# Performance work log

Measured on AMD Instinct MI355X. Metric: run time of the kernel, lower is better.

Reference implementation:

```python
import jax, jax.numpy as jnp
import numpy as np

B, C, H, W = 512, 128, 7, 7
P = 21            # patch_size
DIL = 2           # dilation_patch
PAD = DIL * (P // 2)  # 20: max displacement in pixels


def setup_inputs() -> dict:
    key = jax.random.key(0)
    k1, k2, k3, k4 = jax.random.split(key, 4)
    patch1 = jax.random.normal(k1, (B, C, H, W), jnp.float32)
    patch2 = jax.random.normal(k2, (B, C, H, W), jnp.float32)
    feat = P * P * H * W  # 21609
    w_bbox = jax.random.normal(k3, (4, feat), jnp.float32) * (1.0 / np.sqrt(feat))
    b_bbox = jax.random.normal(k4, (4,), jnp.float32) * 0.01
    return {"patch1": patch1, "patch2": patch2, "w_bbox": w_bbox, "b_bbox": b_bbox}


def _correlation(patch1, patch2):
    """SpatialCorrelationSampler(patch_size=21, dilation_patch=2, kernel_size=1).

    out[b,p,q,i,j] = sum_c patch1[b,c,i,j] * patch2[b,c, i + 2*(p-10), j + 2*(q-10)]
    with zero padding for out-of-bounds displacements. Output: [B, 21, 21, 7, 7].
    """
    padded = jnp.pad(patch2, ((0, 0), (0, 0), (PAD, PAD), (PAD, PAD)))  # [B,C,47,47]
    # Outer product over spatial positions, contracted over channels:
    # T[b,i,j,u,v] = sum_c patch1[b,c,i,j] * padded[b,c,u,v]
    T = jnp.einsum('bcij,bcuv->bijuv', patch1, padded)  # [B,7,7,47,47]
    # Gather the displaced entries: u = 2p + i, v = 2q + j
    Pp, Qq, Ii, Jj = jnp.meshgrid(jnp.arange(P), jnp.arange(P),
                                  jnp.arange(H), jnp.arange(W), indexing='ij')
    corr = T[:, Ii, Jj, DIL * Pp + Ii, DIL * Qq + Jj]  # [B,21,21,7,7]
    return corr


def reference(patch1, patch2, w_bbox, b_bbox):
    corr = _correlation(patch1, patch2)           # [B,21,21,7,7]
    x = corr.reshape(corr.shape[0], -1)           # flatten(start_dim=1)
    return x @ w_bbox.T + b_bbox                  # [B,4]
```

## Files before the change

kernel.cpp:

```cpp
#include <hip/hip_runtime.h>

#define NB    512
#define NC    128
#define HW    49
#define FEAT  21609
#define NPAIR 625
#define CHW   6272
#define NVEC4 1568

__constant__ int c_pi[25]  = {0,0,0,0, 1,1,1, 2,2,2,2, 3,3,3, 4,4,4,4, 5,5,5, 6,6,6,6};
__constant__ int c_pi2[25] = {0,2,4,6, 1,3,5, 0,2,4,6, 1,3,5, 0,2,4,6, 1,3,5, 0,2,4,6};

__global__ __launch_bounds__(256) void corr_head_kernel(
    const float* __restrict__ patch1,
    const float* __restrict__ patch2,
    const float* __restrict__ w_bbox,
    const float* __restrict__ b_bbox,
    float* __restrict__ out)
{
    __shared__ float  s1[CHW];
    __shared__ float  s2[CHW];
    __shared__ float4 s_w[NPAIR];
    __shared__ int    s_pair[NPAIR];
    __shared__ float  s_red[16];

    const int tid = threadIdx.x;
    const int b   = blockIdx.x;

    const float4* g1 = (const float4*)(patch1 + (size_t)b * CHW);
    const float4* g2 = (const float4*)(patch2 + (size_t)b * CHW);
    float4* v1 = (float4*)s1;
    float4* v2 = (float4*)s2;
    for (int t = tid; t < NVEC4; t += 256) {
        v1[t] = g1[t];
        v2[t] = g2[t];
    }

    for (int n = tid; n < NPAIR; n += 256) {
        int a  = n / 25;
        int bb = n - a * 25;
        int i  = c_pi[a],  i2 = c_pi2[a];
        int j  = c_pi[bb], j2 = c_pi2[bb];
        int p  = 10 + ((i2 - i) >> 1);
        int q  = 10 + ((j2 - j) >> 1);
        int feat = ((p * 21 + q) * 7 + i) * 7 + j;
        s_pair[n] = ((i * 7 + j) << 8) | (i2 * 7 + j2);
        s_w[n] = make_float4(w_bbox[feat],
                             w_bbox[FEAT + feat],
                             w_bbox[2 * FEAT + feat],
                             w_bbox[3 * FEAT + feat]);
    }
    __syncthreads();

    float a0 = 0.f, a1 = 0.f, a2 = 0.f, a3 = 0.f;
    for (int n = tid; n < NPAIR; n += 256) {
        int pr = s_pair[n];
        int ij = pr >> 8;
        int kl = pr & 255;
        const float* p1c = s1 + ij;
        const float* p2c = s2 + kl;
        float dot = 0.f;
        #pragma unroll 16
        for (int c = 0; c < NC; ++c)
            dot += p1c[c * HW] * p2c[c * HW];
        float4 w = s_w[n];
        a0 += dot * w.x;
        a1 += dot * w.y;
        a2 += dot * w.z;
        a3 += dot * w.w;
    }

    for (int off = 32; off > 0; off >>= 1) {
        a0 += __shfl_down(a0, off, 64);
        a1 += __shfl_down(a1, off, 64);
        a2 += __shfl_down(a2, off, 64);
        a3 += __shfl_down(a3, off, 64);
    }
    int wave = tid >> 6;
    if ((tid & 63) == 0) {
        s_red[wave * 4 + 0] = a0;
        s_red[wave * 4 + 1] = a1;
        s_red[wave * 4 + 2] = a2;
        s_red[wave * 4 + 3] = a3;
    }
    __syncthreads();
    if (tid < 4) {
        float r = s_red[tid] + s_red[4 + tid] + s_red[8 + tid] + s_red[12 + tid];
        out[b * 4 + tid] = r + b_bbox[tid];
    }
}

extern "C" void kernel_launch(void* const* d_in, const int* in_sizes, int n_in,
                              void* d_out, int out_size, void* d_ws, size_t ws_size,
                              hipStream_t stream) {
    const float* patch1 = (const float*)d_in[0];
    const float* patch2 = (const float*)d_in[1];
    const float* w_bbox = (const float*)d_in[2];
    const float* b_bbox = (const float*)d_in[3];
    float* out = (float*)d_out;
    corr_head_kernel<<<dim3(NB), dim3(256), 0, stream>>>(patch1, patch2, w_bbox, b_bbox, out);
}
```

Baseline: 80.39 us.

## Transpose patches to channel-contiguous smem and split channels across lanes

```diff
diff --git a/kernel.cpp b/kernel.cpp
--- a/kernel.cpp
+++ b/kernel.cpp
@@ -4,12 +4,11 @@
 #define NC    128
 #define HW    49
 #define FEAT  21609
-#define NPAIR 625
 #define CHW   6272
-#define NVEC4 1568
+#define NV4   1568
+#define TSTR  132
 
-__constant__ int c_pi[25]  = {0,0,0,0, 1,1,1, 2,2,2,2, 3,3,3, 4,4,4,4, 5,5,5, 6,6,6,6};
-__constant__ int c_pi2[25] = {0,2,4,6, 1,3,5, 0,2,4,6, 1,3,5, 0,2,4,6, 1,3,5, 0,2,4,6};
+__constant__ int c_S[7] = {0, 4, 7, 11, 14, 18, 21};
 
 __global__ __launch_bounds__(256) void corr_head_kernel(
     const float* __restrict__ patch1,
@@ -18,56 +17,78 @@
     const float* __restrict__ b_bbox,
     float* __restrict__ out)
 {
-    __shared__ float  s1[CHW];
-    __shared__ float  s2[CHW];
-    __shared__ float4 s_w[NPAIR];
-    __shared__ int    s_pair[NPAIR];
+    __shared__ float  s1t[HW * TSTR];
+    __shared__ float  s2t[HW * TSTR];
+    __shared__ float4 s_w[625];
     __shared__ float  s_red[16];
 
     const int tid = threadIdx.x;
     const int b   = blockIdx.x;
 
+    if (tid < 49) {
+        int i  = tid / 7, j = tid - 7 * i;
+        int ci = 4 - (i & 1);
+        int n  = c_S[i] * 25 + ci * c_S[j];
+        for (int i2 = (i & 1); i2 < 7; i2 += 2) {
+            for (int j2 = (j & 1); j2 < 7; j2 += 2) {
+                int p = 10 + ((i2 - i) >> 1);
+                int q = 10 + ((j2 - j) >> 1);
+                int f = ((p * 21 + q) * 7 + i) * 7 + j;
+                s_w[n] = make_float4(w_bbox[f], w_bbox[FEAT + f],
+                                     w_bbox[2 * FEAT + f], w_bbox[3 * FEAT + f]);
+                ++n;
+            }
+        }
+    }
+
     const float4* g1 = (const float4*)(patch1 + (size_t)b * CHW);
     const float4* g2 = (const float4*)(patch2 + (size_t)b * CHW);
-    float4* v1 = (float4*)s1;
-    float4* v2 = (float4*)s2;
-    for (int t = tid; t < NVEC4; t += 256) {
-        v1[t] = g1[t];
-        v2[t] = g2[t];
+    for (int t = tid; t < NV4; t += 256) {
+        float4 v = g1[t];
+        int e = t * 4;
+        #pragma unroll
+        for (int k = 0; k < 4; ++k) {
+            int ee = e + k;
+            int c  = ee / 49;
+            int ij = ee - 49 * c;
+            s1t[ij * TSTR + c] = (&v.x)[k];
+        }
     }
-
-    for (int n = tid; n < NPAIR; n += 256) {
-        int a  = n / 25;
-        int bb = n - a * 25;
-        int i  = c_pi[a],  i2 = c_pi2[a];
-        int j  = c_pi[bb], j2 = c_pi2[bb];
-        int p  = 10 + ((i2 - i) >> 1);
-        int q  = 10 + ((j2 - j) >> 1);
-        int feat = ((p * 21 + q) * 7 + i) * 7 + j;
-        s_pair[n] = ((i * 7 + j) << 8) | (i2 * 7 + j2);
-        s_w[n] = make_float4(w_bbox[feat],
-                             w_bbox[FEAT + feat],
-                             w_bbox[2 * FEAT + feat],
-                             w_bbox[3 * FEAT + feat]);
+    for (int t = tid; t < NV4; t += 256) {
+        float4 v = g2[t];
+        int e = t * 4;
+        #pragma unroll
+        for (int k = 0; k < 4; ++k) {
+            int ee = e + k;
+            int c  = ee / 49;
+            int ij = ee - 49 * c;
+            s2t[ij * TSTR + c] = (&v.x)[k];
+        }
     }
     __syncthreads();
 
+    const int p  = tid >> 5;
+    const int co = (tid & 31) * 4;
     float a0 = 0.f, a1 = 0.f, a2 = 0.f, a3 = 0.f;
-    for (int n = tid; n < NPAIR; n += 256) {
-        int pr = s_pair[n];
-        int ij = pr >> 8;
-        int kl = pr & 255;
-        const float* p1c = s1 + ij;
-        const float* p2c = s2 + kl;
-        float dot = 0.f;
-        #pragma unroll 16
-        for (int c = 0; c < NC; ++c)
-            dot += p1c[c * HW] * p2c[c * HW];
-        float4 w = s_w[n];
-        a0 += dot * w.x;
-        a1 += dot * w.y;
-        a2 += dot * w.z;
-        a3 += dot * w.w;
+
+    for (int ij = p; ij < 49; ij += 8) {
+        int i = ij / 7, j = ij - 7 * i;
+        const float4 f1 = *(const float4*)(s1t + ij * TSTR + co);
+        int ci = 4 - (i & 1);
+        int n  = c_S[i] * 25 + ci * c_S[j];
+        for (int i2 = (i & 1); i2 < 7; i2 += 2) {
+            const float* rowb = s2t + (i2 * 7) * TSTR + co;
+            for (int j2 = (j & 1); j2 < 7; j2 += 2) {
+                const float4 f2 = *(const float4*)(rowb + j2 * TSTR);
+                float4 w4 = s_w[n];
+                ++n;
+                float s = f1.x * f2.x + f1.y * f2.y + f1.z * f2.z + f1.w * f2.w;
+                a0 = fmaf(s, w4.x, a0);
+                a1 = fmaf(s, w4.y, a1);
+                a2 = fmaf(s, w4.z, a2);
+                a3 = fmaf(s, w4.w, a3);
+            }
+        }
     }
 
     for (int off = 32; off > 0; off >>= 1) {
@@ -76,12 +97,12 @@
         a2 += __shfl_down(a2, off, 64);
         a3 += __shfl_down(a3, off, 64);
     }
-    int wave = tid >> 6;
     if ((tid & 63) == 0) {
-        s_red[wave * 4 + 0] = a0;
-        s_red[wave * 4 + 1] = a1;
-        s_red[wave * 4 + 2] = a2;
-        s_red[wave * 4 + 3] = a3;
+        int w = tid >> 6;
+        s_red[w * 4 + 0] = a0;
+        s_red[w * 4 + 1] = a1;
+        s_red[w * 4 + 2] = a2;
+        s_red[w * 4 + 3] = a3;
     }
     __syncthreads();
     if (tid < 4) {
```

After: 88.60 us. 10.2% more time.
